# Optimization experiments

Hardware: AMD Instinct MI355X
Metric: run time of the kernel (lower is better)

## Reference

```python
import jax, jax.numpy as jnp
import numpy as np

NUM_GRAPHS = 1000


def gcn_conv(x, src, dst, n_nodes, W, b):
    """PyG GCNConv: symmetric normalization with self-loops, then scatter-add."""
    # self-loops already appended to src/dst by caller
    deg = jax.ops.segment_sum(jnp.ones_like(dst, dtype=x.dtype), dst, num_segments=n_nodes)
    dinv = jnp.where(deg > 0, jax.lax.rsqrt(deg), 0.0)
    norm = dinv[src] * dinv[dst]                      # [E+N]
    h = x @ W.T                                       # [N, out]
    msg = h[src] * norm[:, None]                      # gather + scale
    out = jax.ops.segment_sum(msg, dst, num_segments=n_nodes)
    return out + b


def setup_inputs() -> dict:
    key = jax.random.key(0)
    ks = jax.random.split(key, 9)
    N, E = 100000, 1600000
    x = jax.random.normal(ks[0], (N, 32), dtype=jnp.float32)
    edge_index = jax.random.randint(ks[1], (2, E), 0, N, dtype=jnp.int64)
    batch = jnp.sort(jax.random.randint(ks[2], (N,), 0, NUM_GRAPHS, dtype=jnp.int64))
    # parameters (Glorot-ish scale)
    W1 = jax.random.normal(ks[3], (16, 32), dtype=jnp.float32) * (1.0 / np.sqrt(32))
    b1 = jnp.zeros((16,), dtype=jnp.float32)
    W2 = jax.random.normal(ks[4], (16, 16), dtype=jnp.float32) * (1.0 / np.sqrt(16))
    b2 = jnp.zeros((16,), dtype=jnp.float32)
    Wl = jax.random.normal(ks[5], (5, 16), dtype=jnp.float32) * (1.0 / np.sqrt(16))
    bl = jnp.zeros((5,), dtype=jnp.float32)
    return {"x": x, "edge_index": edge_index, "batch": batch,
            "W1": W1, "b1": b1, "W2": W2, "b2": b2, "Wl": Wl, "bl": bl}


def reference(x, edge_index, batch, W1, b1, W2, b2, Wl, bl):
    n_nodes = x.shape[0]
    loops = jnp.arange(n_nodes, dtype=edge_index.dtype)
    src = jnp.concatenate([edge_index[0], loops])
    dst = jnp.concatenate([edge_index[1], loops])

    h = gcn_conv(x, src, dst, n_nodes, W1, b1)
    h = jax.nn.relu(h)
    h = gcn_conv(h, src, dst, n_nodes, W2, b2)

    # global mean pool over graphs
    sums = jax.ops.segment_sum(h, batch, num_segments=NUM_GRAPHS)
    cnts = jax.ops.segment_sum(jnp.ones((n_nodes,), dtype=h.dtype), batch, num_segments=NUM_GRAPHS)
    pooled = sums / jnp.maximum(cnts, 1.0)[:, None]   # [G, 16]

    logits = pooled @ Wl.T + bl                       # [G, 5]
    return jax.nn.softmax(logits, axis=-1)
```

## Files before the change

### kernel.cpp

```cpp
#include <hip/hip_runtime.h>
#include <hip/hip_fp16.h>
#include <math.h>

#define NG 1000
#define NPN 512
#define PSH 9
#define MAXPART 256
#define K1BLK 256

__global__ void __launch_bounds__(256) hist_kernel(const int* __restrict__ dst,
                                                   int* __restrict__ bhist,
                                                   int4* __restrict__ zero4, int z4,
                                                   int E, int CH) {
    __shared__ int h[MAXPART];
    int b = blockIdx.x, t = threadIdx.x;
    h[t] = 0;
    int gid = b * 256 + t;
    if (gid < z4) zero4[gid] = make_int4(0, 0, 0, 0);
    __syncthreads();
    int beg = b * CH, end = min(E, beg + CH);
    for (int e = beg + t; e < end; e += 256) atomicAdd(&h[dst[e] >> PSH], 1);
    __syncthreads();
    bhist[b * MAXPART + t] = h[t];
}

__global__ void __launch_bounds__(256) scan_kernel(const int* __restrict__ bhist,
                                                   int* __restrict__ gbase,
                                                   int* __restrict__ poff,
                                                   int* __restrict__ rowptr,
                                                   int NPART, int N, int E) {
    __shared__ int sm[256];
    int t = threadIdx.x;
    int running = 0;
    for (int b = 0; b < K1BLK; b++) {
        int v = bhist[b * MAXPART + t];
        gbase[b * MAXPART + t] = running;
        running += v;
    }
    sm[t] = running;
    __syncthreads();
    for (int o = 1; o < 256; o <<= 1) {
        int u = (t >= o) ? sm[t - o] : 0;
        __syncthreads();
        sm[t] += u;
        __syncthreads();
    }
    int ex = sm[t] - running;
    if (t < NPART) poff[t] = ex;
    if (t == NPART - 1) poff[NPART] = ex + running;
    if (t == 0) rowptr[N] = E;
}

__global__ void __launch_bounds__(256) scatter_kernel(const int* __restrict__ src,
                                                      const int* __restrict__ dst,
                                                      const int* __restrict__ poff,
                                                      const int* __restrict__ gbase,
                                                      int* __restrict__ ibuf,
                                                      int E, int CH, int NPART) {
    __shared__ int cur[MAXPART];
    int b = blockIdx.x, t = threadIdx.x;
    if (t < NPART) cur[t] = poff[t] + gbase[b * MAXPART + t];
    __syncthreads();
    int beg = b * CH, end = min(E, beg + CH);
    for (int e = beg + t; e < end; e += 256) {
        int s = src[e], d = dst[e];
        int p = d >> PSH;
        int pos = atomicAdd(&cur[p], 1);
        ibuf[pos] = ((d & (NPN - 1)) << 17) | s;
    }
}

__global__ void __launch_bounds__(256) part_kernel(const int* __restrict__ poff,
                                                   const int* __restrict__ ibuf,
                                                   int* __restrict__ csr,
                                                   int* __restrict__ rowptr,
                                                   float* __restrict__ dinv,
                                                   const float* __restrict__ X,
                                                   const float* __restrict__ W1,
                                                   __half* __restrict__ A1h, int N) {
    __shared__ int h[NPN];
    __shared__ int ex[NPN];
    __shared__ int cur[NPN];
    __shared__ int sm[256];
    __shared__ float sW1[512];
    int p = blockIdx.x, t = threadIdx.x;
    int base = p * NPN;
    for (int k = t; k < NPN; k += 256) h[k] = 0;
    sW1[t] = W1[t];
    sW1[t + 256] = W1[t + 256];
    __syncthreads();
    int ebeg = poff[p], eend = poff[p + 1];
    for (int e = ebeg + t; e < eend; e += 256) atomicAdd(&h[ibuf[e] >> 17], 1);
    __syncthreads();
    int a0 = h[2 * t], a1 = h[2 * t + 1];
    int s = a0 + a1;
    sm[t] = s;
    __syncthreads();
    for (int o = 1; o < 256; o <<= 1) {
        int u = (t >= o) ? sm[t - o] : 0;
        __syncthreads();
        sm[t] += u;
        __syncthreads();
    }
    int exc = sm[t] - s;
    ex[2 * t] = exc;          cur[2 * t] = exc;
    ex[2 * t + 1] = exc + a0; cur[2 * t + 1] = exc + a0;
    __syncthreads();
    for (int k = t; k < NPN; k += 256) {
        int n = base + k;
        if (n < N) {
            rowptr[n] = ebeg + ex[k];
            dinv[n] = rsqrtf((float)h[k] + 1.0f);
        }
    }
    for (int e = ebeg + t; e < eend; e += 256) {
        int w = ibuf[e];
        int ln = w >> 17;
        int pos = ebeg + atomicAdd(&cur[ln], 1);
        csr[pos] = w & 0x1FFFF;
    }
    for (int k = t; k < NPN; k += 256) {
        int n = base + k;
        if (n >= N) continue;
        float dd = rsqrtf((float)h[k] + 1.0f);
        float xv[32];
        const float4* xp = (const float4*)(X + (size_t)n * 32);
#pragma unroll
        for (int qq = 0; qq < 8; qq++) {
            float4 v = xp[qq];
            xv[4*qq+0] = v.x; xv[4*qq+1] = v.y; xv[4*qq+2] = v.z; xv[4*qq+3] = v.w;
        }
        union { __half2 h2[8]; uint4 u4[2]; } pk;
#pragma unroll
        for (int j2 = 0; j2 < 8; j2++) {
            float o[2];
#pragma unroll
            for (int jj = 0; jj < 2; jj++) {
                int j = j2 * 2 + jj;
                float a = 0.f;
#pragma unroll
                for (int kk = 0; kk < 32; kk++) a += xv[kk] * sW1[j * 32 + kk];
                o[jj] = a * dd;
            }
            pk.h2[j2] = __floats2half2_rn(o[0], o[1]);
        }
        uint4* yp = (uint4*)(A1h + (size_t)n * 16);
        yp[0] = pk.u4[0];
        yp[1] = pk.u4[1];
    }
}

__device__ __forceinline__ void add8(float* a, uint4 v) {
    float2 f;
    f = __half22float2(*(const __half2*)&v.x); a[0] += f.x; a[1] += f.y;
    f = __half22float2(*(const __half2*)&v.y); a[2] += f.x; a[3] += f.y;
    f = __half22float2(*(const __half2*)&v.z); a[4] += f.x; a[5] += f.y;
    f = __half22float2(*(const __half2*)&v.w); a[6] += f.x; a[7] += f.y;
}

__global__ void __launch_bounds__(256) agg1_kernel(
    const int* __restrict__ rowptr, const int* __restrict__ csr,
    const float* __restrict__ dinv, const __half* __restrict__ A1h,
    const float* __restrict__ b1, const float* __restrict__ W2,
    __half* __restrict__ A2h, int N) {
    __shared__ float sW2[256];
    __shared__ float sb1[16];
    __shared__ float tile[128][17];
    int t = threadIdx.x;
    int team = t >> 1, q = t & 1;
    int node = blockIdx.x * 128 + team;
    sW2[t] = W2[t];
    if (t < 16) sb1[t] = b1[t];
    __syncthreads();
    const uint4* H4 = (const uint4*)A1h;
    float dd = 0.f;
    if (node < N) {
        dd = dinv[node];
        float acc[8] = {0.f,0.f,0.f,0.f,0.f,0.f,0.f,0.f};
        add8(acc, H4[(size_t)node * 2 + q]);
        int e = rowptr[node], end = rowptr[node + 1];
        for (; e + 3 < end; e += 4) {
            int s0 = csr[e], s1 = csr[e+1], s2 = csr[e+2], s3 = csr[e+3];
            uint4 g0 = H4[(size_t)s0 * 2 + q];
            uint4 g1 = H4[(size_t)s1 * 2 + q];
            uint4 g2 = H4[(size_t)s2 * 2 + q];
            uint4 g3 = H4[(size_t)s3 * 2 + q];
            add8(acc, g0); add8(acc, g1); add8(acc, g2); add8(acc, g3);
        }
        for (; e < end; e++) add8(acc, H4[(size_t)csr[e] * 2 + q]);
#pragma unroll
        for (int j = 0; j < 8; j++)
            tile[team][q * 8 + j] = fmaxf(acc[j] * dd + sb1[q * 8 + j], 0.f);
    }
    __syncthreads();
    if (node < N) {
        float o[8];
#pragma unroll
        for (int jj = 0; jj < 8; jj++) {
            int j = q * 8 + jj;
            float a = 0.f;
#pragma unroll
            for (int k = 0; k < 16; k++) a += tile[team][k] * sW2[j * 16 + k];
            o[jj] = a * dd;
        }
        uint4 ov;
        ((__half2*)&ov)[0] = __floats2half2_rn(o[0], o[1]);
        ((__half2*)&ov)[1] = __floats2half2_rn(o[2], o[3]);
        ((__half2*)&ov)[2] = __floats2half2_rn(o[4], o[5]);
        ((__half2*)&ov)[3] = __floats2half2_rn(o[6], o[7]);
        ((uint4*)A2h)[(size_t)node * 2 + q] = ov;
    }
}

__global__ void __launch_bounds__(256) agg2_kernel(
    const int* __restrict__ rowptr, const int* __restrict__ csr,
    const float* __restrict__ dinv, const __half* __restrict__ A2h,
    const int* __restrict__ batch, float* __restrict__ pooled,
    float* __restrict__ cnt, int N) {
    __shared__ float tile[128][17];
    __shared__ int gb[128];
    int t = threadIdx.x;
    int team = t >> 1, q = t & 1;
    int base = blockIdx.x * 128;
    int node = base + team;
    if (t < 128) {
        int n = base + t;
        gb[t] = (n < N) ? batch[n] : -1;
    }
    const uint4* H4 = (const uint4*)A2h;
    if (node < N) {
        float dd = dinv[node];
        float acc[8] = {0.f,0.f,0.f,0.f,0.f,0.f,0.f,0.f};
        add8(acc, H4[(size_t)node * 2 + q]);
        int e = rowptr[node], end = rowptr[node + 1];
        for (; e + 3 < end; e += 4) {
            int s0 = csr[e], s1 = csr[e+1], s2 = csr[e+2], s3 = csr[e+3];
            uint4 g0 = H4[(size_t)s0 * 2 + q];
            uint4 g1 = H4[(size_t)s1 * 2 + q];
            uint4 g2 = H4[(size_t)s2 * 2 + q];
            uint4 g3 = H4[(size_t)s3 * 2 + q];
            add8(acc, g0); add8(acc, g1); add8(acc, g2); add8(acc, g3);
        }
        for (; e < end; e++) add8(acc, H4[(size_t)csr[e] * 2 + q]);
#pragma unroll
        for (int j = 0; j < 8; j++) tile[team][q * 8 + j] = acc[j] * dd;
    }
    __syncthreads();
    int nmax = N - base; if (nmax > 128) nmax = 128;
    if (t < 16 && nmax > 0) {
        int c = t;
        int g = gb[0];
        float a = 0.f, k = 0.f;
        for (int n = 0; n < nmax; n++) {
            int gi = gb[n];
            if (gi != g) {
                atomicAdd(&pooled[(size_t)g * 16 + c], a);
                if (c == 0) atomicAdd(&cnt[g], k);
                a = 0.f; k = 0.f; g = gi;
            }
            a += tile[n][c];
            k += 1.f;
        }
        atomicAdd(&pooled[(size_t)g * 16 + c], a);
        if (c == 0) atomicAdd(&cnt[g], k);
    }
}

__global__ void head_kernel(const float* __restrict__ pooled, const float* __restrict__ cnt,
                            const float* __restrict__ b2, const float* __restrict__ Wl,
                            const float* __restrict__ bl, float* __restrict__ out) {
    int g = blockIdx.x * blockDim.x + threadIdx.x;
    if (g >= NG) return;
    float c = cnt[g];
    c = c > 1.0f ? c : 1.0f;
    float inv = 1.0f / c;
    float p[16];
#pragma unroll
    for (int j = 0; j < 16; j++) p[j] = pooled[(size_t)g * 16 + j] * inv + b2[j];
    float logits[5], m = -INFINITY;
#pragma unroll
    for (int r = 0; r < 5; r++) {
        float a = bl[r];
#pragma unroll
        for (int j = 0; j < 16; j++) a += p[j] * Wl[r * 16 + j];
        logits[r] = a;
        m = fmaxf(m, a);
    }
    float s = 0.f;
#pragma unroll
    for (int r = 0; r < 5; r++) { logits[r] = expf(logits[r] - m); s += logits[r]; }
    float is = 1.0f / s;
#pragma unroll
    for (int r = 0; r < 5; r++) out[(size_t)g * 5 + r] = logits[r] * is;
}

static inline size_t rnd16b(size_t bytes) { return (bytes + 15) & ~(size_t)15; }

extern "C" void kernel_launch(void* const* d_in, const int* in_sizes, int n_in,
                              void* d_out, int out_size, void* d_ws, size_t ws_size,
                              hipStream_t stream) {
    const float* x     = (const float*)d_in[0];
    const int*   edge  = (const int*)d_in[1];
    const int*   batch = (const int*)d_in[2];
    const float* W1    = (const float*)d_in[3];
    const float* b1    = (const float*)d_in[4];
    const float* W2    = (const float*)d_in[5];
    const float* b2    = (const float*)d_in[6];
    const float* Wl    = (const float*)d_in[7];
    const float* bl    = (const float*)d_in[8];

    const int N = in_sizes[0] / 32;
    const int E = in_sizes[1] / 2;
    const int* src = edge;
    const int* dst = edge + E;

    const int NPART = (N + NPN - 1) / NPN;
    const int CH = (E + K1BLK - 1) / K1BLK;

    char* ws = (char*)d_ws;
    size_t off = 0;
    float*    pooled = (float*)(ws + off);    off += rnd16b((size_t)NG * 16 * 4);
    float*    cnt    = (float*)(ws + off);    off += rnd16b((size_t)NG * 4);
    size_t zbytes = off;
    int*      poff   = (int*)(ws + off);      off += rnd16b((size_t)(MAXPART + 1) * 4);
    int*      rowptr = (int*)(ws + off);      off += rnd16b((size_t)(N + 1) * 4);
    float*    dinv   = (float*)(ws + off);    off += rnd16b((size_t)N * 4);
    int*      bhist  = (int*)(ws + off);      off += rnd16b((size_t)K1BLK * MAXPART * 4);
    int*      gbase  = (int*)(ws + off);      off += rnd16b((size_t)K1BLK * MAXPART * 4);
    int*      ibuf   = (int*)(ws + off);      off += rnd16b((size_t)E * 4);
    int*      csr    = (int*)(ws + off);      off += rnd16b((size_t)E * 4);
    __half*   A1h    = (__half*)(ws + off);   off += rnd16b((size_t)N * 16 * 2);
    __half*   A2h    = (__half*)(ws + off);   off += rnd16b((size_t)N * 16 * 2);

    int z4 = (int)(zbytes / 16);

    hist_kernel<<<K1BLK, 256, 0, stream>>>(dst, bhist, (int4*)d_ws, z4, E, CH);
    scan_kernel<<<1, 256, 0, stream>>>(bhist, gbase, poff, rowptr, NPART, N, E);
    scatter_kernel<<<K1BLK, 256, 0, stream>>>(src, dst, poff, gbase, ibuf, E, CH, NPART);
    part_kernel<<<NPART, 256, 0, stream>>>(poff, ibuf, csr, rowptr, dinv, x, W1, A1h, N);

    int gAgg = (N + 127) / 128;
    agg1_kernel<<<gAgg, 256, 0, stream>>>(rowptr, csr, dinv, A1h, b1, W2, A2h, N);
    agg2_kernel<<<gAgg, 256, 0, stream>>>(rowptr, csr, dinv, A2h, batch, pooled, cnt, N);
    head_kernel<<<(NG + 255) / 256, 256, 0, stream>>>(pooled, cnt, b2, Wl, bl, (float*)d_out);
}
```

Measured before the change: 109.1 us.

## Parallelize partition offset scan across wavefronts with transposed histogram layout

Replaces the single-block scan, which walked 256 block histograms serially per partition, with a two-stage scan. The histogram is stored transposed so that each wavefront scans one partition's 256 block counts using shuffles, and a small second kernel scans the per-partition totals. This removes a long serial loop on one workgroup, at the cost of one extra kernel launch and a small scratch buffer.

Measured after the change: 103.1 us (median of 2 runs). -5.4%, faster.

```diff
diff --git a/kernel.cpp b/kernel.cpp
--- a/kernel.cpp
+++ b/kernel.cpp
@@ -21,34 +21,59 @@
     int beg = b * CH, end = min(E, beg + CH);
     for (int e = beg + t; e < end; e += 256) atomicAdd(&h[dst[e] >> PSH], 1);
     __syncthreads();
-    bhist[b * MAXPART + t] = h[t];
-}
-
-__global__ void __launch_bounds__(256) scan_kernel(const int* __restrict__ bhist,
-                                                   int* __restrict__ gbase,
+    bhist[t * K1BLK + b] = h[t];
+}
+
+__global__ void __launch_bounds__(256) scanA_kernel(const int* __restrict__ bhist,
+                                                    int* __restrict__ gbase,
+                                                    int* __restrict__ pcnt, int NPART) {
+    int wid = blockIdx.x * 4 + (threadIdx.x >> 6);
+    int lane = threadIdx.x & 63;
+    if (wid >= NPART) return;
+    int base = wid * K1BLK + lane * 4;
+    int v0 = bhist[base + 0], v1 = bhist[base + 1];
+    int v2 = bhist[base + 2], v3 = bhist[base + 3];
+    int s = v0 + v1 + v2 + v3;
+    int incl = s;
+    for (int off = 1; off < 64; off <<= 1) {
+        int u = __shfl_up(incl, off);
+        if (lane >= off) incl += u;
+    }
+    int run = incl - s;
+    gbase[base + 0] = run;            run += v0;
+    gbase[base + 1] = run;            run += v1;
+    gbase[base + 2] = run;            run += v2;
+    gbase[base + 3] = run;
+    if (lane == 63) pcnt[wid] = incl;
+}
+
+__global__ void __launch_bounds__(64) scanB_kernel(const int* __restrict__ pcnt,
                                                    int* __restrict__ poff,
                                                    int* __restrict__ rowptr,
                                                    int NPART, int N, int E) {
-    __shared__ int sm[256];
-    int t = threadIdx.x;
-    int running = 0;
-    for (int b = 0; b < K1BLK; b++) {
-        int v = bhist[b * MAXPART + t];
-        gbase[b * MAXPART + t] = running;
-        running += v;
-    }
-    sm[t] = running;
-    __syncthreads();
-    for (int o = 1; o < 256; o <<= 1) {
-        int u = (t >= o) ? sm[t - o] : 0;
-        __syncthreads();
-        sm[t] += u;
-        __syncthreads();
-    }
-    int ex = sm[t] - running;
-    if (t < NPART) poff[t] = ex;
-    if (t == NPART - 1) poff[NPART] = ex + running;
-    if (t == 0) rowptr[N] = E;
+    int lane = threadIdx.x;
+    int v[4];
+    int s = 0;
+#pragma unroll
+    for (int k = 0; k < 4; k++) {
+        int idx = lane * 4 + k;
+        v[k] = (idx < NPART) ? pcnt[idx] : 0;
+        s += v[k];
+    }
+    int incl = s;
+    for (int off = 1; off < 64; off <<= 1) {
+        int u = __shfl_up(incl, off);
+        if (lane >= off) incl += u;
+    }
+    int run = incl - s;
+#pragma unroll
+    for (int k = 0; k < 4; k++) {
+        int idx = lane * 4 + k;
+        if (idx < NPART) poff[idx] = run;
+        run += v[k];
+    }
+    int grand = __shfl(incl, 63);
+    if (lane == 0) { poff[NPART] = grand; rowptr[N] = E; }
 }
 
 __global__ void __launch_bounds__(256) scatter_kernel(const int* __restrict__ src,
@@ -59,7 +84,7 @@
                                                       int E, int CH, int NPART) {
     __shared__ int cur[MAXPART];
     int b = blockIdx.x, t = threadIdx.x;
-    if (t < NPART) cur[t] = poff[t] + gbase[b * MAXPART + t];
+    if (t < NPART) cur[t] = poff[t] + gbase[t * K1BLK + b];
     __syncthreads();
     int beg = b * CH, end = min(E, beg + CH);
     for (int e = beg + t; e < end; e += 256) {
@@ -323,6 +348,7 @@
     float*    cnt    = (float*)(ws + off);    off += rnd16b((size_t)NG * 4);
     size_t zbytes = off;
     int*      poff   = (int*)(ws + off);      off += rnd16b((size_t)(MAXPART + 1) * 4);
+    int*      pcnt   = (int*)(ws + off);      off += rnd16b((size_t)MAXPART * 4);
     int*      rowptr = (int*)(ws + off);      off += rnd16b((size_t)(N + 1) * 4);
     float*    dinv   = (float*)(ws + off);    off += rnd16b((size_t)N * 4);
     int*      bhist  = (int*)(ws + off);      off += rnd16b((size_t)K1BLK * MAXPART * 4);
@@ -335,7 +361,8 @@
     int z4 = (int)(zbytes / 16);
 
     hist_kernel<<<K1BLK, 256, 0, stream>>>(dst, bhist, (int4*)d_ws, z4, E, CH);
-    scan_kernel<<<1, 256, 0, stream>>>(bhist, gbase, poff, rowptr, NPART, N, E);
+    scanA_kernel<<<(NPART + 3) / 4, 256, 0, stream>>>(bhist, gbase, pcnt, NPART);
+    scanB_kernel<<<1, 64, 0, stream>>>(pcnt, poff, rowptr, NPART, N, E);
     scatter_kernel<<<K1BLK, 256, 0, stream>>>(src, dst, poff, gbase, ibuf, E, CH, NPART);
     part_kernel<<<NPART, 256, 0, stream>>>(poff, ibuf, csr, rowptr, dinv, x, W1, A1h, N);
 
```
